# Optimization experiments

Hardware: AMD Instinct MI355X
Metric: run time of the kernel (lower is better)

Reference implementation:

```python
import jax, jax.numpy as jnp
import numpy as np

PH = PW = 5  # roi_size
EPS = 1e-5


def _conv1x1(x, w, b):
    # x: (B,Cin,H,W), w: (Cout,Cin)
    return jnp.einsum('bchw,oc->bohw', x, w) + b[None, :, None, None]


def _resize_ac(x, oh, ow):
    # F.interpolate bilinear, align_corners=True. x: (B,C,H,W)
    B, C, H, W = x.shape
    ys = jnp.linspace(0.0, H - 1.0, oh)
    xs = jnp.linspace(0.0, W - 1.0, ow)
    y0 = jnp.floor(ys).astype(jnp.int32); y1 = jnp.minimum(y0 + 1, H - 1)
    x0 = jnp.floor(xs).astype(jnp.int32); x1 = jnp.minimum(x0 + 1, W - 1)
    ly = (ys - y0)[:, None]; lx = (xs - x0)[None, :]
    v00 = x[:, :, y0[:, None], x0[None, :]]
    v01 = x[:, :, y0[:, None], x1[None, :]]
    v10 = x[:, :, y1[:, None], x0[None, :]]
    v11 = x[:, :, y1[:, None], x1[None, :]]
    return v00 * (1 - ly) * (1 - lx) + v01 * (1 - ly) * lx + v10 * ly * (1 - lx) + v11 * ly * lx


def _roi_align_one(feat, box):
    # torchvision RoIAlign, spatial_scale=1, sampling_ratio=1, aligned=False
    # feat: (C,H,W), box: (x1,y1,x2,y2)
    C, H, W = feat.shape
    bx1, by1, bx2, by2 = box[0], box[1], box[2], box[3]
    rw = jnp.maximum(bx2 - bx1, 1.0)
    rh = jnp.maximum(by2 - by1, 1.0)
    xs = bx1 + (jnp.arange(PW, dtype=feat.dtype) + 0.5) * (rw / PW)
    ys = by1 + (jnp.arange(PH, dtype=feat.dtype) + 0.5) * (rh / PH)
    yg = jnp.broadcast_to(ys[:, None], (PH, PW))
    xg = jnp.broadcast_to(xs[None, :], (PH, PW))
    valid = (yg >= -1.0) & (yg <= H) & (xg >= -1.0) & (xg <= W)
    y = jnp.clip(yg, 0.0, H - 1.0); x = jnp.clip(xg, 0.0, W - 1.0)
    y0 = jnp.floor(y).astype(jnp.int32); x0 = jnp.floor(x).astype(jnp.int32)
    y1i = jnp.minimum(y0 + 1, H - 1); x1i = jnp.minimum(x0 + 1, W - 1)
    ly = y - y0; lx = x - x0
    v = (feat[:, y0, x0] * (1 - ly) * (1 - lx) + feat[:, y0, x1i] * (1 - ly) * lx
         + feat[:, y1i, x0] * ly * (1 - lx) + feat[:, y1i, x1i] * ly * lx)
    return v * valid  # (C,PH,PW)


def _layernorm(x, w, b):
    mu = jnp.mean(x, -1, keepdims=True)
    var = jnp.var(x, -1, keepdims=True)
    return (x - mu) * jax.lax.rsqrt(var + EPS) * w + b


def setup_inputs() -> dict:
    key = jax.random.key(0)
    ks = jax.random.split(key, 16)
    B, G, NB, HF = 8, 8, 16, 28
    x4 = jax.random.normal(ks[0], (B, 1024, 14, 14), jnp.float32)
    x5 = jax.random.normal(ks[1], (B, 2048, 7, 7), jnp.float32)
    bx = jax.random.uniform(ks[2], (B, NB), minval=0.0, maxval=18.0)
    by = jax.random.uniform(ks[3], (B, NB), minval=0.0, maxval=18.0)
    bw = jax.random.uniform(ks[4], (B, NB), minval=3.0, maxval=10.0)
    bh = jax.random.uniform(ks[5], (B, NB), minval=3.0, maxval=10.0)
    boxes = jnp.stack([bx, by, jnp.minimum(bx + bw, 28.0), jnp.minimum(by + bh, 28.0)], -1)
    group = jax.random.randint(ks[6], (B, G, 2), 0, NB, jnp.int32)
    real_in_num = jnp.full((B,), G, jnp.int32)
    label_s = jax.random.randint(ks[7], (B, G), 0, 6, jnp.int64)
    label_s = jnp.where(jnp.arange(G)[None, :] % 3 == 0, -1, label_s)  # exercise both branches
    skeleton = jax.random.normal(ks[8], (B, G, HF, HF), jnp.float32)
    D = 1536 * PH * PW  # 38400
    return {
        'x4': x4, 'x5': x5, 'boxes': boxes, 'skeleton': skeleton,
        'group': group, 'real_in_num': real_in_num, 'label_s': label_s,
        'conv1_w': jax.random.normal(ks[9], (), jnp.float32) * 0.5,
        'conv1_b': jax.random.normal(ks[10], (), jnp.float32) * 0.1,
        'conv2_w': jax.random.normal(ks[11], (512, 1024), jnp.float32) * 0.03,
        'conv2_b': jnp.zeros((512,), jnp.float32),
        'conv3_w': jax.random.normal(ks[12], (1024, 2048), jnp.float32) * 0.02,
        'conv3_b': jnp.zeros((1024,), jnp.float32),
        'norm1_w': jnp.ones((D,), jnp.float32), 'norm1_b': jnp.zeros((D,), jnp.float32),
        'norm2_w': jnp.ones((512,), jnp.float32), 'norm2_b': jnp.zeros((512,), jnp.float32),
        'fc1_w': jax.random.normal(ks[13], (512, D), jnp.float32) * float(np.sqrt(2.0 / D)),
        'fc1_b': jnp.zeros((512,), jnp.float32),
        'fc2_w': jax.random.normal(ks[14], (6, 512), jnp.float32) * float(np.sqrt(2.0 / 512)),
        'fc2_b': jnp.zeros((6,), jnp.float32),
    }


def reference(x4, x5, boxes, skeleton, group, real_in_num, label_s,
              conv1_w, conv1_b, conv2_w, conv2_b, conv3_w, conv3_b,
              norm1_w, norm1_b, norm2_w, norm2_b, fc1_w, fc1_b, fc2_w, fc2_b):
    B, G = skeleton.shape[0], skeleton.shape[1]
    HF, WF = skeleton.shape[2], skeleton.shape[3]
    # backbone heads: 1x1 conv + bilinear upsample (align_corners=True), concat
    f4 = _resize_ac(_conv1x1(x4, conv2_w, conv2_b), HF, WF)   # (B,512,28,28)
    f5 = _resize_ac(_conv1x1(x5, conv3_w, conv3_b), HF, WF)   # (B,1024,28,28)
    app = jnp.concatenate([f4, f5], axis=1)                   # (B,1536,28,28)
    C = app.shape[1]
    # per-person pose gate: 1x1 conv (scalar on single channel) + sigmoid
    gate = jax.nn.sigmoid(skeleton * conv1_w + conv1_b)       # (B,G,28,28)
    gated = gate[:, :, None] * app[:, None]                   # (B,G,C,28,28)
    use_gate = (label_s != -1)[:, :, None, None, None]
    pose_feature = jnp.where(use_gate, gated, app[:, None])   # (B,G,C,28,28)
    # union box of the two interacting people (get_box_tensor)
    bidx = jnp.arange(B)[:, None]
    b1 = boxes[bidx, group[..., 0]]                           # (B,G,4)
    b2 = boxes[bidx, group[..., 1]]
    ub = jnp.stack([jnp.minimum(b1[..., 0], b2[..., 0]), jnp.minimum(b1[..., 1], b2[..., 1]),
                    jnp.maximum(b1[..., 2], b2[..., 2]), jnp.maximum(b1[..., 3], b2[..., 3])], -1)
    # batched RoIAlign over all N = B*G boxes
    feats = pose_feature.reshape(B * G, C, HF, WF)
    rois = jax.vmap(_roi_align_one)(feats, ub.reshape(B * G, 4))  # (N,C,5,5)
    sk = rois.reshape(B * G, -1)                              # (N,38400)
    sk = jax.nn.relu(_layernorm(sk, norm1_w, norm1_b))
    # dropout(p=0.9) is identity in eval mode
    sk = sk @ fc1_w.T + fc1_b
    sk = _layernorm(sk, norm2_w, norm2_b)
    score = sk @ fc2_w.T + fc2_b                              # (N,6)
    return score
```

## Files before the change

### kernel.cpp

```cpp
#include <hip/hip_runtime.h>
#include <math.h>

#define B8   8
#define HW4  196
#define HW5  49
#define HFW  28
#define NPIX 784
#define CAPP 1536
#define D1   38400
#define NR   64

typedef short short8 __attribute__((ext_vector_type(8)));
typedef short short4v __attribute__((ext_vector_type(4)));
typedef float floatx16 __attribute__((ext_vector_type(16)));

__device__ __forceinline__ unsigned short f2bf(float f) {
  unsigned u = __float_as_uint(f);
  u += 0x7FFF + ((u >> 16) & 1);
  return (unsigned short)(u >> 16);
}

__global__ __launch_bounds__(256) void tt_kernel(
    const float* __restrict__ x4, const float* __restrict__ x5,
    unsigned short* __restrict__ x4T, unsigned short* __restrict__ x5T) {
  __shared__ float tile[64 * 201];
  int blk = blockIdx.x, t = threadIdx.x;
  if (blk < 128) {
    int b = blk >> 4, cc = blk & 15;
    for (int i = t; i < 64 * HW4; i += 256) {
      int c = i / HW4, hw = i - c * HW4;
      tile[c * 201 + hw] = x4[((size_t)(b * 1024 + cc * 64 + c)) * HW4 + hw];
    }
    __syncthreads();
    for (int i = t; i < HW4 * 64; i += 256) {
      int hw = i >> 6, c = i & 63;
      x4T[((size_t)(b * HW4 + hw)) * 1024 + cc * 64 + c] = f2bf(tile[c * 201 + hw]);
    }
  } else {
    int blk2 = blk - 128;
    int b = blk2 >> 5, cc = blk2 & 31;
    for (int i = t; i < 64 * HW5; i += 256) {
      int c = i / HW5, hw = i - c * HW5;
      tile[c * 51 + hw] = x5[((size_t)(b * 2048 + cc * 64 + c)) * HW5 + hw];
    }
    __syncthreads();
    for (int i = t; i < HW5 * 64; i += 256) {
      int hw = i >> 6, c = i & 63;
      x5T[((size_t)(b * HW5 + hw)) * 2048 + cc * 64 + c] = f2bf(tile[c * 51 + hw]);
    }
  }
}

__global__ __launch_bounds__(256) void gemm_kernel(
    const unsigned short* __restrict__ A, const float* __restrict__ Bw,
    float* __restrict__ C,
    int mtiles, int ntiles, int Mvalid, int N, int K, int kchunk) {
  __shared__ unsigned short As[2][8][64][8];
  __shared__ unsigned short Bs[2][8][64][8];
  int bid = blockIdx.x;
  int mt = bid % mtiles; int rest = bid / mtiles;
  int nt = rest % ntiles; int sp = rest / ntiles;
  int k0 = sp * kchunk;
  int nkb = kchunk >> 6;
  int t = threadIdx.x;
  int wave = t >> 6, lane = t & 63;
  int wm = wave & 1, wn = wave >> 1;

  const unsigned short* Aptr = A + (size_t)(mt * 64) * K + k0;
  const float* Bptr = Bw + (size_t)(nt * 64) * K + k0;

  short8 areg[2];
  float4 breg[4];

  floatx16 acc;
#pragma unroll
  for (int i = 0; i < 16; i++) acc[i] = 0.f;

#pragma unroll
  for (int i = 0; i < 2; i++) {
    int e = t + i * 256;
    areg[i] = *(const short8*)(Aptr + (size_t)(e >> 3) * K + (e & 7) * 8);
  }
#pragma unroll
  for (int i = 0; i < 4; i++) {
    int e = t + i * 256;
    breg[i] = *(const float4*)(Bptr + (size_t)(e >> 4) * K + (e & 15) * 4);
  }
#pragma unroll
  for (int i = 0; i < 2; i++) {
    int e = t + i * 256;
    *(short8*)&As[0][e & 7][e >> 3][0] = areg[i];
  }
#pragma unroll
  for (int i = 0; i < 4; i++) {
    int e = t + i * 256;
    short4v v;
    v[0] = (short)f2bf(breg[i].x); v[1] = (short)f2bf(breg[i].y);
    v[2] = (short)f2bf(breg[i].z); v[3] = (short)f2bf(breg[i].w);
    *(short4v*)&Bs[0][(e & 15) >> 1][e >> 4][((e & 15) & 1) * 4] = v;
  }
  __syncthreads();

  for (int kb = 0; kb < nkb; kb++) {
    int buf = kb & 1;
    bool more = (kb + 1) < nkb;
    if (more) {
      int kof = (kb + 1) * 64;
#pragma unroll
      for (int i = 0; i < 2; i++) {
        int e = t + i * 256;
        areg[i] = *(const short8*)(Aptr + (size_t)(e >> 3) * K + kof + (e & 7) * 8);
      }
#pragma unroll
      for (int i = 0; i < 4; i++) {
        int e = t + i * 256;
        breg[i] = *(const float4*)(Bptr + (size_t)(e >> 4) * K + kof + (e & 15) * 4);
      }
    }
#pragma unroll
    for (int s = 0; s < 4; s++) {
      short8 af = *(const short8*)&As[buf][2 * s + (lane >> 5)][wm * 32 + (lane & 31)][0];
      short8 bf = *(const short8*)&Bs[buf][2 * s + (lane >> 5)][wn * 32 + (lane & 31)][0];
      acc = __builtin_amdgcn_mfma_f32_32x32x16_bf16(af, bf, acc, 0, 0, 0);
    }
    __syncthreads();
    if (more) {
      int nb = 1 - buf;
#pragma unroll
      for (int i = 0; i < 2; i++) {
        int e = t + i * 256;
        *(short8*)&As[nb][e & 7][e >> 3][0] = areg[i];
      }
#pragma unroll
      for (int i = 0; i < 4; i++) {
        int e = t + i * 256;
        short4v v;
        v[0] = (short)f2bf(breg[i].x); v[1] = (short)f2bf(breg[i].y);
        v[2] = (short)f2bf(breg[i].z); v[3] = (short)f2bf(breg[i].w);
        *(short4v*)&Bs[nb][(e & 15) >> 1][e >> 4][((e & 15) & 1) * 4] = v;
      }
      __syncthreads();
    }
  }

  int col = nt * 64 + wn * 32 + (lane & 31);
  int rbase = mt * 64 + wm * 32 + 4 * (lane >> 5);
#pragma unroll
  for (int reg = 0; reg < 16; reg++) {
    int row = rbase + (reg & 3) + 8 * (reg >> 2);
    if (row < Mvalid) atomicAdd(&C[(size_t)row * N + col], acc[reg]);
  }
}

__device__ __forceinline__ float gate_val(const float* sk, int yy, int xx,
                                          float c1w, float c1b, bool use) {
  if (!use) return 1.f;
  float z = sk[yy * HFW + xx] * c1w + c1b;
  return 1.f / (1.f + expf(-z));
}

__global__ __launch_bounds__(256) void prep_kernel(
    const float* __restrict__ boxes, const int* __restrict__ group,
    const int* __restrict__ label, const float* __restrict__ skel,
    const float* __restrict__ c1w_, const float* __restrict__ c1b_,
    float* __restrict__ descw, int* __restrict__ desco,
    float* __restrict__ tap4w, int* __restrict__ tap4o,
    float* __restrict__ tap5w, int* __restrict__ tap5o) {
  int blk = blockIdx.x, t = threadIdx.x;
  if (blk < 64) {
    int bg = blk, p = t;
    if (p >= 25) return;
    int b = bg >> 3;
    int i1 = group[bg * 2 + 0], i2 = group[bg * 2 + 1];
    const float* bb1 = boxes + (size_t)(b * 16 + i1) * 4;
    const float* bb2 = boxes + (size_t)(b * 16 + i2) * 4;
    float ux1 = fminf(bb1[0], bb2[0]);
    float uy1 = fminf(bb1[1], bb2[1]);
    float ux2 = fmaxf(bb1[2], bb2[2]);
    float uy2 = fmaxf(bb1[3], bb2[3]);
    float rw = fmaxf(ux2 - ux1, 1.0f), rh = fmaxf(uy2 - uy1, 1.0f);
    int iy = p / 5, ix = p % 5;
    float sy = uy1 + (iy + 0.5f) * (rh * 0.2f);
    float sx = ux1 + (ix + 0.5f) * (rw * 0.2f);
    float valid = (sy >= -1.0f && sy <= 28.0f && sx >= -1.0f && sx <= 28.0f) ? 1.f : 0.f;
    float y = fminf(fmaxf(sy, 0.f), 27.f);
    float x = fminf(fmaxf(sx, 0.f), 27.f);
    int y0 = (int)floorf(y), x0 = (int)floorf(x);
    int y1 = min(y0 + 1, 27), x1 = min(x0 + 1, 27);
    float ly = y - (float)y0, lx = x - (float)x0;
    bool use = (label[bg] != -1);
    float c1w = c1w_[0], c1b = c1b_[0];
    const float* sk = skel + (size_t)bg * NPIX;
    int idx = (bg * 25 + p) * 4;
    descw[idx + 0] = (1.f - ly) * (1.f - lx) * valid * gate_val(sk, y0, x0, c1w, c1b, use);
    descw[idx + 1] = (1.f - ly) * lx * valid * gate_val(sk, y0, x1, c1w, c1b, use);
    descw[idx + 2] = ly * (1.f - lx) * valid * gate_val(sk, y1, x0, c1w, c1b, use);
    descw[idx + 3] = ly * lx * valid * gate_val(sk, y1, x1, c1w, c1b, use);
    desco[idx + 0] = y0 * HFW + x0;
    desco[idx + 1] = y0 * HFW + x1;
    desco[idx + 2] = y1 * HFW + x0;
    desco[idx + 3] = y1 * HFW + x1;
  } else {
    int pix = (blk - 64) * 196 + t;
    if (t >= 196) return;
    int y = pix / HFW, x = pix % HFW;
    {
      float sy = y * (13.0f / 27.0f), sx = x * (13.0f / 27.0f);
      int y0 = (int)sy, x0 = (int)sx;
      int y1 = min(y0 + 1, 13), x1 = min(x0 + 1, 13);
      float ly = sy - y0, lx = sx - x0;
      tap4o[pix * 4 + 0] = y0 * 14 + x0; tap4w[pix * 4 + 0] = (1.f - ly) * (1.f - lx);
      tap4o[pix * 4 + 1] = y0 * 14 + x1; tap4w[pix * 4 + 1] = (1.f - ly) * lx;
      tap4o[pix * 4 + 2] = y1 * 14 + x0; tap4w[pix * 4 + 2] = ly * (1.f - lx);
      tap4o[pix * 4 + 3] = y1 * 14 + x1; tap4w[pix * 4 + 3] = ly * lx;
    }
    {
      float sy = y * (6.0f / 27.0f), sx = x * (6.0f / 27.0f);
      int y0 = (int)sy, x0 = (int)sx;
      int y1 = min(y0 + 1, 6), x1 = min(x0 + 1, 6);
      float ly = sy - y0, lx = sx - x0;
      tap5o[pix * 4 + 0] = y0 * 7 + x0; tap5w[pix * 4 + 0] = (1.f - ly) * (1.f - lx);
      tap5o[pix * 4 + 1] = y0 * 7 + x1; tap5w[pix * 4 + 1] = (1.f - ly) * lx;
      tap5o[pix * 4 + 2] = y1 * 7 + x0; tap5w[pix * 4 + 2] = ly * (1.f - lx);
      tap5o[pix * 4 + 3] = y1 * 7 + x1; tap5w[pix * 4 + 3] = ly * lx;
    }
  }
}

__global__ __launch_bounds__(256) void roi_kernel(
    const float* __restrict__ f4T, const float* __restrict__ f5T,
    const float* __restrict__ descw, const int* __restrict__ desco,
    const float* __restrict__ tap4w, const int* __restrict__ tap4o,
    const float* __restrict__ tap5w, const int* __restrict__ tap5o,
    const float* __restrict__ b4, const float* __restrict__ b5,
    float* __restrict__ roisP, float* __restrict__ stats) {
  int p = blockIdx.x, bg = blockIdx.y, b = bg >> 3, t = threadIdx.x;
  __shared__ float cw4[16], cw5[16], wgs;
  __shared__ int co4[16], co5[16];
  int di = (bg * 25 + p) * 4;
  if (t < 16) {
    int i = t >> 2, j = t & 3;
    float wg = descw[di + i];
    int pix = desco[di + i];
    cw4[t] = wg * tap4w[pix * 4 + j];
    co4[t] = (b * HW4 + tap4o[pix * 4 + j]) * 512;
    cw5[t] = wg * tap5w[pix * 4 + j];
    co5[t] = (b * HW5 + tap5o[pix * 4 + j]) * 1024;
  }
  if (t == 16) wgs = descw[di] + descw[di + 1] + descw[di + 2] + descw[di + 3];
  __syncthreads();
  float w4r[16], w5r[16];
  int o4r[16], o5r[16];
  float wg = wgs;
#pragma unroll
  for (int i = 0; i < 16; i++) {
    w4r[i] = cw4[i]; o4r[i] = co4[i];
    w5r[i] = cw5[i]; o5r[i] = co5[i];
  }
  float ls = 0.f, ls2 = 0.f;
  float* outp = roisP + (size_t)(bg * 25 + p) * CAPP;
  for (int c = t; c < 512; c += 256) {
    float acc = wg * b4[c];
#pragma unroll
    for (int i = 0; i < 16; i++) acc = fmaf(w4r[i], f4T[o4r[i] + c], acc);
    outp[c] = acc;
    ls += acc; ls2 = fmaf(acc, acc, ls2);
  }
  for (int c = t; c < 1024; c += 256) {
    float acc = wg * b5[c];
#pragma unroll
    for (int i = 0; i < 16; i++) acc = fmaf(w5r[i], f5T[o5r[i] + c], acc);
    outp[512 + c] = acc;
    ls += acc; ls2 = fmaf(acc, acc, ls2);
  }
  for (int off = 32; off; off >>= 1) {
    ls += __shfl_down(ls, off);
    ls2 += __shfl_down(ls2, off);
  }
  __shared__ float red[8];
  int wv = t >> 6;
  if ((t & 63) == 0) { red[wv] = ls; red[4 + wv] = ls2; }
  __syncthreads();
  if (t == 0) {
    atomicAdd(&stats[bg * 2 + 0], red[0] + red[1] + red[2] + red[3]);
    atomicAdd(&stats[bg * 2 + 1], red[4] + red[5] + red[6] + red[7]);
  }
}

__global__ __launch_bounds__(256) void ln1b_kernel(
    const float* __restrict__ roisP, const float* __restrict__ stats,
    const float* __restrict__ n1w, const float* __restrict__ n1b,
    unsigned short* __restrict__ sknT) {
  int o = blockIdx.x * 256 + threadIdx.x;
  int r = o / D1;
  int k = o - r * D1;
  unsigned c = (unsigned)k / 25u;
  unsigned p = (unsigned)k - c * 25u;
  float x = roisP[((size_t)(r * 25 + p)) * CAPP + c];
  float S = stats[r * 2], S2 = stats[r * 2 + 1];
  float mu = S * (1.f / D1);
  float var = S2 * (1.f / D1) - mu * mu;
  float rs = rsqrtf(var + 1e-5f);
  float v = fmaf((x - mu) * rs, n1w[k], n1b[k]);
  sknT[o] = f2bf(fmaxf(v, 0.f));
}

__global__ __launch_bounds__(256) void ln2fc2_kernel(
    const float* __restrict__ out1, const float* __restrict__ b1,
    const float* __restrict__ n2w, const float* __restrict__ n2b,
    const float* __restrict__ w2, const float* __restrict__ b2,
    float* __restrict__ out) {
  int r = blockIdx.x, t = threadIdx.x;
  int j1 = t, j2 = t + 256;
  float v1 = out1[r * 512 + j1] + b1[j1];
  float v2 = out1[r * 512 + j2] + b1[j2];
  float s = v1 + v2, s2 = v1 * v1 + v2 * v2;
  for (int off = 32; off; off >>= 1) {
    s += __shfl_down(s, off);
    s2 += __shfl_down(s2, off);
  }
  __shared__ float red[8];
  int wv = t >> 6;
  if ((t & 63) == 0) { red[wv] = s; red[4 + wv] = s2; }
  __syncthreads();
  float S = red[0] + red[1] + red[2] + red[3];
  float S2 = red[4] + red[5] + red[6] + red[7];
  float mu = S / 512.f;
  float var = S2 / 512.f - mu * mu;
  float rs = rsqrtf(var + 1e-5f);
  float n1v = fmaf((v1 - mu) * rs, n2w[j1], n2b[j1]);
  float n2v = fmaf((v2 - mu) * rs, n2w[j2], n2b[j2]);
  float pm[6];
#pragma unroll
  for (int m = 0; m < 6; m++)
    pm[m] = n1v * w2[m * 512 + j1] + n2v * w2[m * 512 + j2];
#pragma unroll
  for (int m = 0; m < 6; m++)
    for (int off = 32; off; off >>= 1) pm[m] += __shfl_down(pm[m], off);
  __shared__ float red2[24];
  if ((t & 63) == 0) {
#pragma unroll
    for (int m = 0; m < 6; m++) red2[wv * 6 + m] = pm[m];
  }
  __syncthreads();
  if (t < 6)
    out[r * 6 + t] = red2[t] + red2[6 + t] + red2[12 + t] + red2[18 + t] + b2[t];
}

extern "C" void kernel_launch(void* const* d_in, const int* in_sizes, int n_in,
                              void* d_out, int out_size, void* d_ws, size_t ws_size,
                              hipStream_t stream) {
  const float* x4    = (const float*)d_in[0];
  const float* x5    = (const float*)d_in[1];
  const float* boxes = (const float*)d_in[2];
  const float* skel  = (const float*)d_in[3];
  const int*   group = (const int*)d_in[4];
  const int*   label = (const int*)d_in[6];
  const float* c1w   = (const float*)d_in[7];
  const float* c1b   = (const float*)d_in[8];
  const float* w2c   = (const float*)d_in[9];
  const float* b2c   = (const float*)d_in[10];
  const float* w3c   = (const float*)d_in[11];
  const float* b3c   = (const float*)d_in[12];
  const float* n1w   = (const float*)d_in[13];
  const float* n1b   = (const float*)d_in[14];
  const float* n2w   = (const float*)d_in[15];
  const float* n2b   = (const float*)d_in[16];
  const float* fw1   = (const float*)d_in[17];
  const float* fb1   = (const float*)d_in[18];
  const float* fw2   = (const float*)d_in[19];
  const float* fb2   = (const float*)d_in[20];
  float* out = (float*)d_out;

  float* ws = (float*)d_ws;
  unsigned short* x4T = (unsigned short*)ws;
  unsigned short* x5T = (unsigned short*)(ws + 819200);
  float* f4T   = ws + 1277952;
  float* f5T   = ws + 2097152;
  float* tap4w = ws + 2555904;
  int*   tap4o = (int*)(ws + 2559040);
  float* tap5w = ws + 2562176;
  int*   tap5o = (int*)(ws + 2565312);
  float* descw = ws + 2568448;
  int*   desco = (int*)(ws + 2574848);
  float* roisP = ws + 2581248;
  float* stats = ws + 5038848;
  unsigned short* sknT = (unsigned short*)(ws + 5038976);
  float* out1  = ws + 6267776;

  hipMemsetAsync(f4T, 0, 819200 * sizeof(float), stream);
  hipMemsetAsync(f5T, 0, 458752 * sizeof(float), stream);
  hipMemsetAsync(stats, 0, 128 * sizeof(float), stream);
  hipMemsetAsync(out1, 0, 32768 * sizeof(float), stream);

  tt_kernel<<<384, 256, 0, stream>>>(x4, x5, x4T, x5T);
  prep_kernel<<<68, 256, 0, stream>>>(boxes, group, label, skel, c1w, c1b,
                                      descw, desco, tap4w, tap4o, tap5w, tap5o);
  gemm_kernel<<<800, 256, 0, stream>>>(x4T, w2c, f4T, 25, 8, 1568, 512, 1024, 256);
  gemm_kernel<<<896, 256, 0, stream>>>(x5T, w3c, f5T, 7, 16, 392, 1024, 2048, 256);
  roi_kernel<<<dim3(25, NR), 256, 0, stream>>>(f4T, f5T, descw, desco,
                                               tap4w, tap4o, tap5w, tap5o,
                                               b2c, b3c, roisP, stats);
  ln1b_kernel<<<9600, 256, 0, stream>>>(roisP, stats, n1w, n1b, sknT);
  gemm_kernel<<<1200, 256, 0, stream>>>(sknT, fw1, out1, 1, 8, 64, 512, 38400, 256);
  ln2fc2_kernel<<<NR, 256, 0, stream>>>(out1, fb1, n2w, n2b, fw2, fb2, out);
}
```

Before: 267.8 us.

## Fuse all stages into one persistent cooperative kernel with grid syncs

```diff
diff --git a/kernel.cpp b/kernel.cpp
--- a/kernel.cpp
+++ b/kernel.cpp
@@ -1,5 +1,8 @@
 #include <hip/hip_runtime.h>
+#include <hip/hip_cooperative_groups.h>
 #include <math.h>
+
+namespace cg = cooperative_groups;
 
 #define B8   8
 #define HW4  196
@@ -9,6 +12,7 @@
 #define CAPP 1536
 #define D1   38400
 #define NR   64
+#define NTHREADS 65536
 
 typedef short short8 __attribute__((ext_vector_type(8)));
 typedef short short4v __attribute__((ext_vector_type(4)));
@@ -20,61 +24,49 @@
   return (unsigned short)(u >> 16);
 }
 
-__global__ __launch_bounds__(256) void tt_kernel(
-    const float* __restrict__ x4, const float* __restrict__ x5,
-    unsigned short* __restrict__ x4T, unsigned short* __restrict__ x5T) {
-  __shared__ float tile[64 * 201];
-  int blk = blockIdx.x, t = threadIdx.x;
-  if (blk < 128) {
-    int b = blk >> 4, cc = blk & 15;
-    for (int i = t; i < 64 * HW4; i += 256) {
-      int c = i / HW4, hw = i - c * HW4;
-      tile[c * 201 + hw] = x4[((size_t)(b * 1024 + cc * 64 + c)) * HW4 + hw];
-    }
-    __syncthreads();
-    for (int i = t; i < HW4 * 64; i += 256) {
-      int hw = i >> 6, c = i & 63;
-      x4T[((size_t)(b * HW4 + hw)) * 1024 + cc * 64 + c] = f2bf(tile[c * 201 + hw]);
-    }
-  } else {
-    int blk2 = blk - 128;
-    int b = blk2 >> 5, cc = blk2 & 31;
-    for (int i = t; i < 64 * HW5; i += 256) {
-      int c = i / HW5, hw = i - c * HW5;
-      tile[c * 51 + hw] = x5[((size_t)(b * 2048 + cc * 64 + c)) * HW5 + hw];
-    }
-    __syncthreads();
-    for (int i = t; i < HW5 * 64; i += 256) {
-      int hw = i >> 6, c = i & 63;
-      x5T[((size_t)(b * HW5 + hw)) * 2048 + cc * 64 + c] = f2bf(tile[c * 51 + hw]);
-    }
-  }
-}
-
-__global__ __launch_bounds__(256) void gemm_kernel(
-    const unsigned short* __restrict__ A, const float* __restrict__ Bw,
-    float* __restrict__ C,
-    int mtiles, int ntiles, int Mvalid, int N, int K, int kchunk) {
-  __shared__ unsigned short As[2][8][64][8];
-  __shared__ unsigned short Bs[2][8][64][8];
-  int bid = blockIdx.x;
-  int mt = bid % mtiles; int rest = bid / mtiles;
-  int nt = rest % ntiles; int sp = rest / ntiles;
-  int k0 = sp * kchunk;
-  int nkb = kchunk >> 6;
+struct Params {
+  const float *x4, *x5, *boxes, *skel;
+  const int *group, *label;
+  const float *c1w, *c1b, *w2c, *b2c, *w3c, *b3c;
+  const float *n1w, *n1b, *n2w, *n2b, *fw1, *fb1, *fw2, *fb2;
+  float* out;
+  unsigned short *x4T, *x5T, *sknT;
+  float *f4T, *f5T, *tap4w, *tap5w, *descw, *roisP, *stats, *out1;
+  int *tap4o, *tap5o, *desco;
+};
+
+union SharedU {
+  float tile[64 * 201];
+  struct {
+    unsigned short As[2][8][64][8];
+    unsigned short Bs[2][8][64][8];
+  } g;
+  struct {
+    float cw4[16], cw5[16], wgs;
+    int co4[16], co5[16];
+    float red[8];
+  } roi;
+  struct {
+    float red[8];
+    float red2[24];
+  } ln;
+};
+
+__device__ __forceinline__ void gemm_unit(
+    SharedU& sh, const unsigned short* __restrict__ A, const float* __restrict__ Bw,
+    float* __restrict__ C, int mt, int nt, int k0, int kchunk,
+    int K, int N, int Mvalid, bool atomicStore) {
   int t = threadIdx.x;
   int wave = t >> 6, lane = t & 63;
   int wm = wave & 1, wn = wave >> 1;
-
   const unsigned short* Aptr = A + (size_t)(mt * 64) * K + k0;
   const float* Bptr = Bw + (size_t)(nt * 64) * K + k0;
-
   short8 areg[2];
   float4 breg[4];
-
   floatx16 acc;
 #pragma unroll
   for (int i = 0; i < 16; i++) acc[i] = 0.f;
+  int nkb = kchunk >> 6;
 
 #pragma unroll
   for (int i = 0; i < 2; i++) {
@@ -89,7 +81,7 @@
 #pragma unroll
   for (int i = 0; i < 2; i++) {
     int e = t + i * 256;
-    *(short8*)&As[0][e & 7][e >> 3][0] = areg[i];
+    *(short8*)&sh.g.As[0][e & 7][e >> 3][0] = areg[i];
   }
 #pragma unroll
   for (int i = 0; i < 4; i++) {
@@ -97,7 +89,7 @@
     short4v v;
     v[0] = (short)f2bf(breg[i].x); v[1] = (short)f2bf(breg[i].y);
     v[2] = (short)f2bf(breg[i].z); v[3] = (short)f2bf(breg[i].w);
-    *(short4v*)&Bs[0][(e & 15) >> 1][e >> 4][((e & 15) & 1) * 4] = v;
+    *(short4v*)&sh.g.Bs[0][(e & 15) >> 1][e >> 4][((e & 15) & 1) * 4] = v;
   }
   __syncthreads();
 
@@ -119,8 +111,8 @@
     }
 #pragma unroll
     for (int s = 0; s < 4; s++) {
-      short8 af = *(const short8*)&As[buf][2 * s + (lane >> 5)][wm * 32 + (lane & 31)][0];
-      short8 bf = *(const short8*)&Bs[buf][2 * s + (lane >> 5)][wn * 32 + (lane & 31)][0];
+      short8 af = *(const short8*)&sh.g.As[buf][2 * s + (lane >> 5)][wm * 32 + (lane & 31)][0];
+      short8 bf = *(const short8*)&sh.g.Bs[buf][2 * s + (lane >> 5)][wn * 32 + (lane & 31)][0];
       acc = __builtin_amdgcn_mfma_f32_32x32x16_bf16(af, bf, acc, 0, 0, 0);
     }
     __syncthreads();
@@ -129,7 +121,7 @@
 #pragma unroll
       for (int i = 0; i < 2; i++) {
         int e = t + i * 256;
-        *(short8*)&As[nb][e & 7][e >> 3][0] = areg[i];
+        *(short8*)&sh.g.As[nb][e & 7][e >> 3][0] = areg[i];
       }
 #pragma unroll
       for (int i = 0; i < 4; i++) {
@@ -137,7 +129,7 @@
         short4v v;
         v[0] = (short)f2bf(breg[i].x); v[1] = (short)f2bf(breg[i].y);
         v[2] = (short)f2bf(breg[i].z); v[3] = (short)f2bf(breg[i].w);
-        *(short4v*)&Bs[nb][(e & 15) >> 1][e >> 4][((e & 15) & 1) * 4] = v;
+        *(short4v*)&sh.g.Bs[nb][(e & 15) >> 1][e >> 4][((e & 15) & 1) * 4] = v;
       }
       __syncthreads();
     }
@@ -148,7 +140,10 @@
 #pragma unroll
   for (int reg = 0; reg < 16; reg++) {
     int row = rbase + (reg & 3) + 8 * (reg >> 2);
-    if (row < Mvalid) atomicAdd(&C[(size_t)row * N + col], acc[reg]);
+    if (row < Mvalid) {
+      if (atomicStore) atomicAdd(&C[(size_t)row * N + col], acc[reg]);
+      else C[(size_t)row * N + col] = acc[reg];
+    }
   }
 }
 
@@ -159,249 +154,282 @@
   return 1.f / (1.f + expf(-z));
 }
 
-__global__ __launch_bounds__(256) void prep_kernel(
-    const float* __restrict__ boxes, const int* __restrict__ group,
-    const int* __restrict__ label, const float* __restrict__ skel,
-    const float* __restrict__ c1w_, const float* __restrict__ c1b_,
-    float* __restrict__ descw, int* __restrict__ desco,
-    float* __restrict__ tap4w, int* __restrict__ tap4o,
-    float* __restrict__ tap5w, int* __restrict__ tap5o) {
-  int blk = blockIdx.x, t = threadIdx.x;
-  if (blk < 64) {
-    int bg = blk, p = t;
-    if (p >= 25) return;
-    int b = bg >> 3;
-    int i1 = group[bg * 2 + 0], i2 = group[bg * 2 + 1];
-    const float* bb1 = boxes + (size_t)(b * 16 + i1) * 4;
-    const float* bb2 = boxes + (size_t)(b * 16 + i2) * 4;
-    float ux1 = fminf(bb1[0], bb2[0]);
-    float uy1 = fminf(bb1[1], bb2[1]);
-    float ux2 = fmaxf(bb1[2], bb2[2]);
-    float uy2 = fmaxf(bb1[3], bb2[3]);
-    float rw = fmaxf(ux2 - ux1, 1.0f), rh = fmaxf(uy2 - uy1, 1.0f);
-    int iy = p / 5, ix = p % 5;
-    float sy = uy1 + (iy + 0.5f) * (rh * 0.2f);
-    float sx = ux1 + (ix + 0.5f) * (rw * 0.2f);
-    float valid = (sy >= -1.0f && sy <= 28.0f && sx >= -1.0f && sx <= 28.0f) ? 1.f : 0.f;
-    float y = fminf(fmaxf(sy, 0.f), 27.f);
-    float x = fminf(fmaxf(sx, 0.f), 27.f);
-    int y0 = (int)floorf(y), x0 = (int)floorf(x);
-    int y1 = min(y0 + 1, 27), x1 = min(x0 + 1, 27);
-    float ly = y - (float)y0, lx = x - (float)x0;
-    bool use = (label[bg] != -1);
-    float c1w = c1w_[0], c1b = c1b_[0];
-    const float* sk = skel + (size_t)bg * NPIX;
-    int idx = (bg * 25 + p) * 4;
-    descw[idx + 0] = (1.f - ly) * (1.f - lx) * valid * gate_val(sk, y0, x0, c1w, c1b, use);
-    descw[idx + 1] = (1.f - ly) * lx * valid * gate_val(sk, y0, x1, c1w, c1b, use);
-    descw[idx + 2] = ly * (1.f - lx) * valid * gate_val(sk, y1, x0, c1w, c1b, use);
-    descw[idx + 3] = ly * lx * valid * gate_val(sk, y1, x1, c1w, c1b, use);
-    desco[idx + 0] = y0 * HFW + x0;
-    desco[idx + 1] = y0 * HFW + x1;
-    desco[idx + 2] = y1 * HFW + x0;
-    desco[idx + 3] = y1 * HFW + x1;
-  } else {
-    int pix = (blk - 64) * 196 + t;
-    if (t >= 196) return;
-    int y = pix / HFW, x = pix % HFW;
-    {
-      float sy = y * (13.0f / 27.0f), sx = x * (13.0f / 27.0f);
-      int y0 = (int)sy, x0 = (int)sx;
-      int y1 = min(y0 + 1, 13), x1 = min(x0 + 1, 13);
-      float ly = sy - y0, lx = sx - x0;
-      tap4o[pix * 4 + 0] = y0 * 14 + x0; tap4w[pix * 4 + 0] = (1.f - ly) * (1.f - lx);
-      tap4o[pix * 4 + 1] = y0 * 14 + x1; tap4w[pix * 4 + 1] = (1.f - ly) * lx;
-      tap4o[pix * 4 + 2] = y1 * 14 + x0; tap4w[pix * 4 + 2] = ly * (1.f - lx);
-      tap4o[pix * 4 + 3] = y1 * 14 + x1; tap4w[pix * 4 + 3] = ly * lx;
-    }
-    {
-      float sy = y * (6.0f / 27.0f), sx = x * (6.0f / 27.0f);
-      int y0 = (int)sy, x0 = (int)sx;
-      int y1 = min(y0 + 1, 6), x1 = min(x0 + 1, 6);
-      float ly = sy - y0, lx = sx - x0;
-      tap5o[pix * 4 + 0] = y0 * 7 + x0; tap5w[pix * 4 + 0] = (1.f - ly) * (1.f - lx);
-      tap5o[pix * 4 + 1] = y0 * 7 + x1; tap5w[pix * 4 + 1] = (1.f - ly) * lx;
-      tap5o[pix * 4 + 2] = y1 * 7 + x0; tap5w[pix * 4 + 2] = ly * (1.f - lx);
-      tap5o[pix * 4 + 3] = y1 * 7 + x1; tap5w[pix * 4 + 3] = ly * lx;
-    }
-  }
-}
-
-__global__ __launch_bounds__(256) void roi_kernel(
-    const float* __restrict__ f4T, const float* __restrict__ f5T,
-    const float* __restrict__ descw, const int* __restrict__ desco,
-    const float* __restrict__ tap4w, const int* __restrict__ tap4o,
-    const float* __restrict__ tap5w, const int* __restrict__ tap5o,
-    const float* __restrict__ b4, const float* __restrict__ b5,
-    float* __restrict__ roisP, float* __restrict__ stats) {
-  int p = blockIdx.x, bg = blockIdx.y, b = bg >> 3, t = threadIdx.x;
-  __shared__ float cw4[16], cw5[16], wgs;
-  __shared__ int co4[16], co5[16];
-  int di = (bg * 25 + p) * 4;
-  if (t < 16) {
-    int i = t >> 2, j = t & 3;
-    float wg = descw[di + i];
-    int pix = desco[di + i];
-    cw4[t] = wg * tap4w[pix * 4 + j];
-    co4[t] = (b * HW4 + tap4o[pix * 4 + j]) * 512;
-    cw5[t] = wg * tap5w[pix * 4 + j];
-    co5[t] = (b * HW5 + tap5o[pix * 4 + j]) * 1024;
-  }
-  if (t == 16) wgs = descw[di] + descw[di + 1] + descw[di + 2] + descw[di + 3];
-  __syncthreads();
-  float w4r[16], w5r[16];
-  int o4r[16], o5r[16];
-  float wg = wgs;
-#pragma unroll
-  for (int i = 0; i < 16; i++) {
-    w4r[i] = cw4[i]; o4r[i] = co4[i];
-    w5r[i] = cw5[i]; o5r[i] = co5[i];
-  }
-  float ls = 0.f, ls2 = 0.f;
-  float* outp = roisP + (size_t)(bg * 25 + p) * CAPP;
-  for (int c = t; c < 512; c += 256) {
-    float acc = wg * b4[c];
-#pragma unroll
-    for (int i = 0; i < 16; i++) acc = fmaf(w4r[i], f4T[o4r[i] + c], acc);
-    outp[c] = acc;
-    ls += acc; ls2 = fmaf(acc, acc, ls2);
-  }
-  for (int c = t; c < 1024; c += 256) {
-    float acc = wg * b5[c];
-#pragma unroll
-    for (int i = 0; i < 16; i++) acc = fmaf(w5r[i], f5T[o5r[i] + c], acc);
-    outp[512 + c] = acc;
-    ls += acc; ls2 = fmaf(acc, acc, ls2);
-  }
-  for (int off = 32; off; off >>= 1) {
-    ls += __shfl_down(ls, off);
-    ls2 += __shfl_down(ls2, off);
-  }
-  __shared__ float red[8];
-  int wv = t >> 6;
-  if ((t & 63) == 0) { red[wv] = ls; red[4 + wv] = ls2; }
-  __syncthreads();
-  if (t == 0) {
-    atomicAdd(&stats[bg * 2 + 0], red[0] + red[1] + red[2] + red[3]);
-    atomicAdd(&stats[bg * 2 + 1], red[4] + red[5] + red[6] + red[7]);
-  }
-}
-
-__global__ __launch_bounds__(256) void ln1b_kernel(
-    const float* __restrict__ roisP, const float* __restrict__ stats,
-    const float* __restrict__ n1w, const float* __restrict__ n1b,
-    unsigned short* __restrict__ sknT) {
-  int o = blockIdx.x * 256 + threadIdx.x;
-  int r = o / D1;
-  int k = o - r * D1;
-  unsigned c = (unsigned)k / 25u;
-  unsigned p = (unsigned)k - c * 25u;
-  float x = roisP[((size_t)(r * 25 + p)) * CAPP + c];
-  float S = stats[r * 2], S2 = stats[r * 2 + 1];
-  float mu = S * (1.f / D1);
-  float var = S2 * (1.f / D1) - mu * mu;
-  float rs = rsqrtf(var + 1e-5f);
-  float v = fmaf((x - mu) * rs, n1w[k], n1b[k]);
-  sknT[o] = f2bf(fmaxf(v, 0.f));
-}
-
-__global__ __launch_bounds__(256) void ln2fc2_kernel(
-    const float* __restrict__ out1, const float* __restrict__ b1,
-    const float* __restrict__ n2w, const float* __restrict__ n2b,
-    const float* __restrict__ w2, const float* __restrict__ b2,
-    float* __restrict__ out) {
-  int r = blockIdx.x, t = threadIdx.x;
-  int j1 = t, j2 = t + 256;
-  float v1 = out1[r * 512 + j1] + b1[j1];
-  float v2 = out1[r * 512 + j2] + b1[j2];
-  float s = v1 + v2, s2 = v1 * v1 + v2 * v2;
-  for (int off = 32; off; off >>= 1) {
-    s += __shfl_down(s, off);
-    s2 += __shfl_down(s2, off);
-  }
-  __shared__ float red[8];
-  int wv = t >> 6;
-  if ((t & 63) == 0) { red[wv] = s; red[4 + wv] = s2; }
-  __syncthreads();
-  float S = red[0] + red[1] + red[2] + red[3];
-  float S2 = red[4] + red[5] + red[6] + red[7];
-  float mu = S / 512.f;
-  float var = S2 / 512.f - mu * mu;
-  float rs = rsqrtf(var + 1e-5f);
-  float n1v = fmaf((v1 - mu) * rs, n2w[j1], n2b[j1]);
-  float n2v = fmaf((v2 - mu) * rs, n2w[j2], n2b[j2]);
-  float pm[6];
-#pragma unroll
-  for (int m = 0; m < 6; m++)
-    pm[m] = n1v * w2[m * 512 + j1] + n2v * w2[m * 512 + j2];
-#pragma unroll
-  for (int m = 0; m < 6; m++)
-    for (int off = 32; off; off >>= 1) pm[m] += __shfl_down(pm[m], off);
-  __shared__ float red2[24];
-  if ((t & 63) == 0) {
-#pragma unroll
-    for (int m = 0; m < 6; m++) red2[wv * 6 + m] = pm[m];
-  }
-  __syncthreads();
-  if (t < 6)
-    out[r * 6 + t] = red2[t] + red2[6 + t] + red2[12 + t] + red2[18 + t] + b2[t];
+__global__ __launch_bounds__(256, 1) void mega_kernel(Params p) {
+  cg::grid_group grid = cg::this_grid();
+  __shared__ SharedU sh;
+  int bid = blockIdx.x, t = threadIdx.x;
+  int gtid = bid * 256 + t;
+
+  {
+    float4 z4 = make_float4(0.f, 0.f, 0.f, 0.f);
+    for (int i = gtid; i < 458752 / 4; i += NTHREADS) ((float4*)p.f5T)[i] = z4;
+    for (int i = gtid; i < 32768 / 4; i += NTHREADS) ((float4*)p.out1)[i] = z4;
+    if (gtid < 128) p.stats[gtid] = 0.f;
+
+    for (int u = bid; u < 452; u += 256) {
+      __syncthreads();
+      if (u < 128) {
+        int b = u >> 4, cc = u & 15;
+        for (int i = t; i < 64 * HW4; i += 256) {
+          int c = i / HW4, hw = i - c * HW4;
+          sh.tile[c * 201 + hw] = p.x4[((size_t)(b * 1024 + cc * 64 + c)) * HW4 + hw];
+        }
+        __syncthreads();
+        for (int i = t; i < HW4 * 64; i += 256) {
+          int hw = i >> 6, c = i & 63;
+          p.x4T[((size_t)(b * HW4 + hw)) * 1024 + cc * 64 + c] = f2bf(sh.tile[c * 201 + hw]);
+        }
+      } else if (u < 384) {
+        int u2 = u - 128;
+        int b = u2 >> 5, cc = u2 & 31;
+        for (int i = t; i < 64 * HW5; i += 256) {
+          int c = i / HW5, hw = i - c * HW5;
+          sh.tile[c * 51 + hw] = p.x5[((size_t)(b * 2048 + cc * 64 + c)) * HW5 + hw];
+        }
+        __syncthreads();
+        for (int i = t; i < HW5 * 64; i += 256) {
+          int hw = i >> 6, c = i & 63;
+          p.x5T[((size_t)(b * HW5 + hw)) * 2048 + cc * 64 + c] = f2bf(sh.tile[c * 51 + hw]);
+        }
+      } else if (u < 448) {
+        int bg = u - 384;
+        if (t < 25) {
+          int b = bg >> 3;
+          int i1 = p.group[bg * 2 + 0], i2 = p.group[bg * 2 + 1];
+          const float* bb1 = p.boxes + (size_t)(b * 16 + i1) * 4;
+          const float* bb2 = p.boxes + (size_t)(b * 16 + i2) * 4;
+          float ux1 = fminf(bb1[0], bb2[0]);
+          float uy1 = fminf(bb1[1], bb2[1]);
+          float ux2 = fmaxf(bb1[2], bb2[2]);
+          float uy2 = fmaxf(bb1[3], bb2[3]);
+          float rw = fmaxf(ux2 - ux1, 1.0f), rh = fmaxf(uy2 - uy1, 1.0f);
+          int iy = t / 5, ix = t % 5;
+          float sy = uy1 + (iy + 0.5f) * (rh * 0.2f);
+          float sx = ux1 + (ix + 0.5f) * (rw * 0.2f);
+          float valid = (sy >= -1.0f && sy <= 28.0f && sx >= -1.0f && sx <= 28.0f) ? 1.f : 0.f;
+          float y = fminf(fmaxf(sy, 0.f), 27.f);
+          float x = fminf(fmaxf(sx, 0.f), 27.f);
+          int y0 = (int)floorf(y), x0 = (int)floorf(x);
+          int y1 = min(y0 + 1, 27), x1 = min(x0 + 1, 27);
+          float ly = y - (float)y0, lx = x - (float)x0;
+          bool use = (p.label[bg] != -1);
+          float c1w = p.c1w[0], c1b = p.c1b[0];
+          const float* sk = p.skel + (size_t)bg * NPIX;
+          int idx = (bg * 25 + t) * 4;
+          p.descw[idx + 0] = (1.f - ly) * (1.f - lx) * valid * gate_val(sk, y0, x0, c1w, c1b, use);
+          p.descw[idx + 1] = (1.f - ly) * lx * valid * gate_val(sk, y0, x1, c1w, c1b, use);
+          p.descw[idx + 2] = ly * (1.f - lx) * valid * gate_val(sk, y1, x0, c1w, c1b, use);
+          p.descw[idx + 3] = ly * lx * valid * gate_val(sk, y1, x1, c1w, c1b, use);
+          p.desco[idx + 0] = y0 * HFW + x0;
+          p.desco[idx + 1] = y0 * HFW + x1;
+          p.desco[idx + 2] = y1 * HFW + x0;
+          p.desco[idx + 3] = y1 * HFW + x1;
+        }
+      } else {
+        int pix = (u - 448) * 196 + t;
+        if (t < 196) {
+          int y = pix / HFW, x = pix % HFW;
+          {
+            float sy = y * (13.0f / 27.0f), sx = x * (13.0f / 27.0f);
+            int y0 = (int)sy, x0 = (int)sx;
+            int y1 = min(y0 + 1, 13), x1 = min(x0 + 1, 13);
+            float ly = sy - y0, lx = sx - x0;
+            p.tap4o[pix * 4 + 0] = y0 * 14 + x0; p.tap4w[pix * 4 + 0] = (1.f - ly) * (1.f - lx);
+            p.tap4o[pix * 4 + 1] = y0 * 14 + x1; p.tap4w[pix * 4 + 1] = (1.f - ly) * lx;
+            p.tap4o[pix * 4 + 2] = y1 * 14 + x0; p.tap4w[pix * 4 + 2] = ly * (1.f - lx);
+            p.tap4o[pix * 4 + 3] = y1 * 14 + x1; p.tap4w[pix * 4 + 3] = ly * lx;
+          }
+          {
+            float sy = y * (6.0f / 27.0f), sx = x * (6.0f / 27.0f);
+            int y0 = (int)sy, x0 = (int)sx;
+            int y1 = min(y0 + 1, 6), x1 = min(x0 + 1, 6);
+            float ly = sy - y0, lx = sx - x0;
+            p.tap5o[pix * 4 + 0] = y0 * 7 + x0; p.tap5w[pix * 4 + 0] = (1.f - ly) * (1.f - lx);
+            p.tap5o[pix * 4 + 1] = y0 * 7 + x1; p.tap5w[pix * 4 + 1] = (1.f - ly) * lx;
+            p.tap5o[pix * 4 + 2] = y1 * 7 + x0; p.tap5w[pix * 4 + 2] = ly * (1.f - lx);
+            p.tap5o[pix * 4 + 3] = y1 * 7 + x1; p.tap5w[pix * 4 + 3] = ly * lx;
+          }
+        }
+      }
+    }
+  }
+  __threadfence();
+  grid.sync();
+
+  for (int u = bid; u < 424; u += 256) {
+    __syncthreads();
+    if (u < 200) {
+      int mt = u % 25, nt = u / 25;
+      gemm_unit(sh, p.x4T, p.w2c, p.f4T, mt, nt, 0, 1024, 1024, 512, 1568, false);
+    } else {
+      int u2 = u - 200;
+      int mt = u2 % 7, r = u2 / 7;
+      int nt = r & 15, sp = r >> 4;
+      gemm_unit(sh, p.x5T, p.w3c, p.f5T, mt, nt, sp * 1024, 1024, 2048, 1024, 392, true);
+    }
+  }
+  __threadfence();
+  grid.sync();
+
+  for (int u = bid; u < 1600; u += 256) {
+    __syncthreads();
+    int pp = u % 25, bg = u / 25, b = bg >> 3;
+    int di = (bg * 25 + pp) * 4;
+    if (t < 16) {
+      int i = t >> 2, j = t & 3;
+      float wg = p.descw[di + i];
+      int pix = p.desco[di + i];
+      sh.roi.cw4[t] = wg * p.tap4w[pix * 4 + j];
+      sh.roi.co4[t] = (b * HW4 + p.tap4o[pix * 4 + j]) * 512;
+      sh.roi.cw5[t] = wg * p.tap5w[pix * 4 + j];
+      sh.roi.co5[t] = (b * HW5 + p.tap5o[pix * 4 + j]) * 1024;
+    }
+    if (t == 16) sh.roi.wgs = p.descw[di] + p.descw[di + 1] + p.descw[di + 2] + p.descw[di + 3];
+    __syncthreads();
+    float w4r[16], w5r[16];
+    int o4r[16], o5r[16];
+    float wg = sh.roi.wgs;
+#pragma unroll
+    for (int i = 0; i < 16; i++) {
+      w4r[i] = sh.roi.cw4[i]; o4r[i] = sh.roi.co4[i];
+      w5r[i] = sh.roi.cw5[i]; o5r[i] = sh.roi.co5[i];
+    }
+    float ls = 0.f, ls2 = 0.f;
+    float* outp = p.roisP + (size_t)(bg * 25 + pp) * CAPP;
+    for (int c = t; c < 512; c += 256) {
+      float acc = wg * p.b2c[c];
+#pragma unroll
+      for (int i = 0; i < 16; i++) acc = fmaf(w4r[i], p.f4T[o4r[i] + c], acc);
+      outp[c] = acc;
+      ls += acc; ls2 = fmaf(acc, acc, ls2);
+    }
+    for (int c = t; c < 1024; c += 256) {
+      float acc = wg * p.b3c[c];
+#pragma unroll
+      for (int i = 0; i < 16; i++) acc = fmaf(w5r[i], p.f5T[o5r[i] + c], acc);
+      outp[512 + c] = acc;
+      ls += acc; ls2 = fmaf(acc, acc, ls2);
+    }
+    for (int off = 32; off; off >>= 1) {
+      ls += __shfl_down(ls, off);
+      ls2 += __shfl_down(ls2, off);
+    }
+    int wv = t >> 6;
+    if ((t & 63) == 0) { sh.roi.red[wv] = ls; sh.roi.red[4 + wv] = ls2; }
+    __syncthreads();
+    if (t == 0) {
+      atomicAdd(&p.stats[bg * 2 + 0], sh.roi.red[0] + sh.roi.red[1] + sh.roi.red[2] + sh.roi.red[3]);
+      atomicAdd(&p.stats[bg * 2 + 1], sh.roi.red[4] + sh.roi.red[5] + sh.roi.red[6] + sh.roi.red[7]);
+    }
+  }
+  __threadfence();
+  grid.sync();
+
+  for (int o = gtid; o < NR * D1; o += NTHREADS) {
+    int r = o / D1;
+    int k = o - r * D1;
+    unsigned c = (unsigned)k / 25u;
+    unsigned pp = (unsigned)k - c * 25u;
+    float x = p.roisP[((size_t)(r * 25 + pp)) * CAPP + c];
+    float S = p.stats[r * 2], S2 = p.stats[r * 2 + 1];
+    float mu = S * (1.f / D1);
+    float var = S2 * (1.f / D1) - mu * mu;
+    float rs = rsqrtf(var + 1e-5f);
+    float v = fmaf((x - mu) * rs, p.n1w[k], p.n1b[k]);
+    p.sknT[o] = f2bf(fmaxf(v, 0.f));
+  }
+  __threadfence();
+  grid.sync();
+
+  for (int u = bid; u < 320; u += 256) {
+    __syncthreads();
+    int nt = u & 7, sp = u >> 3;
+    gemm_unit(sh, p.sknT, p.fw1, p.out1, 0, nt, sp * 960, 960, 38400, 512, 64, true);
+  }
+  __threadfence();
+  grid.sync();
+
+  if (bid < NR) {
+    int r = bid;
+    int j1 = t, j2 = t + 256;
+    float v1 = p.out1[r * 512 + j1] + p.fb1[j1];
+    float v2 = p.out1[r * 512 + j2] + p.fb1[j2];
+    float s = v1 + v2, s2 = v1 * v1 + v2 * v2;
+    for (int off = 32; off; off >>= 1) {
+      s += __shfl_down(s, off);
+      s2 += __shfl_down(s2, off);
+    }
+    int wv = t >> 6;
+    if ((t & 63) == 0) { sh.ln.red[wv] = s; sh.ln.red[4 + wv] = s2; }
+    __syncthreads();
+    float S = sh.ln.red[0] + sh.ln.red[1] + sh.ln.red[2] + sh.ln.red[3];
+    float S2 = sh.ln.red[4] + sh.ln.red[5] + sh.ln.red[6] + sh.ln.red[7];
+    float mu = S / 512.f;
+    float var = S2 / 512.f - mu * mu;
+    float rs = rsqrtf(var + 1e-5f);
+    float n1v = fmaf((v1 - mu) * rs, p.n2w[j1], p.n2b[j1]);
+    float n2v = fmaf((v2 - mu) * rs, p.n2w[j2], p.n2b[j2]);
+    float pm[6];
+#pragma unroll
+    for (int m = 0; m < 6; m++)
+      pm[m] = n1v * p.fw2[m * 512 + j1] + n2v * p.fw2[m * 512 + j2];
+#pragma unroll
+    for (int m = 0; m < 6; m++)
+      for (int off = 32; off; off >>= 1) pm[m] += __shfl_down(pm[m], off);
+    if ((t & 63) == 0) {
+#pragma unroll
+      for (int m = 0; m < 6; m++) sh.ln.red2[wv * 6 + m] = pm[m];
+    }
+    __syncthreads();
+    if (t < 6)
+      p.out[r * 6 + t] = sh.ln.red2[t] + sh.ln.red2[6 + t] + sh.ln.red2[12 + t] +
+                         sh.ln.red2[18 + t] + p.fb2[t];
+  }
 }
 
 extern "C" void kernel_launch(void* const* d_in, const int* in_sizes, int n_in,
                               void* d_out, int out_size, void* d_ws, size_t ws_size,
                               hipStream_t stream) {
-  const float* x4    = (const float*)d_in[0];
-  const float* x5    = (const float*)d_in[1];
-  const float* boxes = (const float*)d_in[2];
-  const float* skel  = (const float*)d_in[3];
-  const int*   group = (const int*)d_in[4];
-  const int*   label = (const int*)d_in[6];
-  const float* c1w   = (const float*)d_in[7];
-  const float* c1b   = (const float*)d_in[8];
-  const float* w2c   = (const float*)d_in[9];
-  const float* b2c   = (const float*)d_in[10];
-  const float* w3c   = (const float*)d_in[11];
-  const float* b3c   = (const float*)d_in[12];
-  const float* n1w   = (const float*)d_in[13];
-  const float* n1b   = (const float*)d_in[14];
-  const float* n2w   = (const float*)d_in[15];
-  const float* n2b   = (const float*)d_in[16];
-  const float* fw1   = (const float*)d_in[17];
-  const float* fb1   = (const float*)d_in[18];
-  const float* fw2   = (const float*)d_in[19];
-  const float* fb2   = (const float*)d_in[20];
-  float* out = (float*)d_out;
+  Params p;
+  p.x4    = (const float*)d_in[0];
+  p.x5    = (const float*)d_in[1];
+  p.boxes = (const float*)d_in[2];
+  p.skel  = (const float*)d_in[3];
+  p.group = (const int*)d_in[4];
+  p.label = (const int*)d_in[6];
+  p.c1w   = (const float*)d_in[7];
+  p.c1b   = (const float*)d_in[8];
+  p.w2c   = (const float*)d_in[9];
+  p.b2c   = (const float*)d_in[10];
+  p.w3c   = (const float*)d_in[11];
+  p.b3c   = (const float*)d_in[12];
+  p.n1w   = (const float*)d_in[13];
+  p.n1b   = (const float*)d_in[14];
+  p.n2w   = (const float*)d_in[15];
+  p.n2b   = (const float*)d_in[16];
+  p.fw1   = (const float*)d_in[17];
+  p.fb1   = (const float*)d_in[18];
+  p.fw2   = (const float*)d_in[19];
+  p.fb2   = (const float*)d_in[20];
+  p.out   = (float*)d_out;
 
   float* ws = (float*)d_ws;
-  unsigned short* x4T = (unsigned short*)ws;
-  unsigned short* x5T = (unsigned short*)(ws + 819200);
-  float* f4T   = ws + 1277952;
-  float* f5T   = ws + 2097152;
-  float* tap4w = ws + 2555904;
-  int*   tap4o = (int*)(ws + 2559040);
-  float* tap5w = ws + 2562176;
-  int*   tap5o = (int*)(ws + 2565312);
-  float* descw = ws + 2568448;
-  int*   desco = (int*)(ws + 2574848);
-  float* roisP = ws + 2581248;
-  float* stats = ws + 5038848;
-  unsigned short* sknT = (unsigned short*)(ws + 5038976);
-  float* out1  = ws + 6267776;
-
-  hipMemsetAsync(f4T, 0, 819200 * sizeof(float), stream);
-  hipMemsetAsync(f5T, 0, 458752 * sizeof(float), stream);
-  hipMemsetAsync(stats, 0, 128 * sizeof(float), stream);
-  hipMemsetAsync(out1, 0, 32768 * sizeof(float), stream);
-
-  tt_kernel<<<384, 256, 0, stream>>>(x4, x5, x4T, x5T);
-  prep_kernel<<<68, 256, 0, stream>>>(boxes, group, label, skel, c1w, c1b,
-                                      descw, desco, tap4w, tap4o, tap5w, tap5o);
-  gemm_kernel<<<800, 256, 0, stream>>>(x4T, w2c, f4T, 25, 8, 1568, 512, 1024, 256);
-  gemm_kernel<<<896, 256, 0, stream>>>(x5T, w3c, f5T, 7, 16, 392, 1024, 2048, 256);
-  roi_kernel<<<dim3(25, NR), 256, 0, stream>>>(f4T, f5T, descw, desco,
-                                               tap4w, tap4o, tap5w, tap5o,
-                                               b2c, b3c, roisP, stats);
-  ln1b_kernel<<<9600, 256, 0, stream>>>(roisP, stats, n1w, n1b, sknT);
-  gemm_kernel<<<1200, 256, 0, stream>>>(sknT, fw1, out1, 1, 8, 64, 512, 38400, 256);
-  ln2fc2_kernel<<<NR, 256, 0, stream>>>(out1, fb1, n2w, n2b, fw2, fb2, out);
+  p.x4T   = (unsigned short*)ws;
+  p.x5T   = (unsigned short*)(ws + 819200);
+  p.f4T   = ws + 1277952;
+  p.f5T   = ws + 2097152;
+  p.tap4w = ws + 2555904;
+  p.tap4o = (int*)(ws + 2559040);
+  p.tap5w = ws + 2562176;
+  p.tap5o = (int*)(ws + 2565312);
+  p.descw = ws + 2568448;
+  p.desco = (int*)(ws + 2574848);
+  p.roisP = ws + 2581248;
+  p.stats = ws + 5038848;
+  p.sknT  = (unsigned short*)(ws + 5038976);
+  p.out1  = ws + 6267776;
+
+  void* args[] = { (void*)&p };
+  hipLaunchCooperativeKernel((const void*)mega_kernel, dim3(256), dim3(256),
+                             args, 0, stream);
 }
```

New measurement: 576.3 us. 115% more time.
